# Optimization experiments

Measured on AMD Instinct MI355X. Metric: run time of the kernel, lower is better.

The kernel has to match this reference:

```python
import jax, jax.numpy as jnp
import numpy as np

NUM_TILES = 64
TPC = 8            # tiles per cluster
GRID = 16          # spline grid size
EPS = 1e-5


def setup_inputs() -> dict:
    key = jax.random.key(0)
    ks = jax.random.split(key, 6)
    B, S, D, T, DH, G = 2, 1024, 512, NUM_TILES, 128, GRID
    x = jax.random.normal(ks[0], (B, S, D), dtype=jnp.float32)
    gamma = jnp.ones((D,), jnp.float32)
    beta = jnp.zeros((D,), jnp.float32)
    # torch layouts: down.weight [DH, D], up.weight [D, DH]
    Wd = jax.random.normal(ks[1], (T, DH, D), dtype=jnp.float32) * 0.02
    spline_bases = jax.random.normal(ks[2], (T, DH, G), dtype=jnp.float32) * 0.1
    spline_slopes = jax.random.normal(ks[3], (T, DH, G), dtype=jnp.float32) * 0.1
    Wu = jax.random.normal(ks[4], (T, D, DH), dtype=jnp.float32) * 0.02
    scale = jnp.full((T,), 0.1, jnp.float32)
    return {"x": x, "gamma": gamma, "beta": beta, "Wd": Wd,
            "spline_bases": spline_bases, "spline_slopes": spline_slopes,
            "Wu": Wu, "scale": scale}


def reference(x, gamma, beta, Wd, spline_bases, spline_slopes, Wu, scale):
    B, S, D = x.shape
    T, DH, _ = Wd.shape
    C = T // TPC
    N = B * S

    # LayerNorm
    mu = x.mean(-1, keepdims=True)
    var = ((x - mu) ** 2).mean(-1, keepdims=True)
    xn = (x - mu) * jax.lax.rsqrt(var + EPS) * gamma + beta
    xf = xn.reshape(N, D)

    # Signatures (first call: ema == current tile signatures)
    tile_sigs = jnp.sign(Wd.mean(axis=1))                         # [T, D]
    cluster_sigs = jnp.sign(tile_sigs.reshape(C, TPC, D).mean(1))  # [C, D]

    # Hierarchical routing: cluster -> tile
    in_sigs = jnp.sign(xf)                                        # [N, D]
    best_c = jnp.argmax(in_sigs @ cluster_sigs.T, axis=-1)        # [N]
    tile_scores = (in_sigs @ tile_sigs.T).reshape(N, C, TPC)      # [N, C, TPC]
    sc = jnp.take_along_axis(tile_scores, best_c[:, None, None], axis=1)[:, 0, :]
    local_best = jnp.argmax(sc, axis=-1)                          # [N]
    tidx = best_c * TPC + local_best                              # [N]

    # Dispatch: gather per-token expert weights, down-project
    h = jnp.einsum('nd,nhd->nh', xf, Wd[tidx])                    # [N, DH]

    # Spline nonlinearity
    hn = jax.nn.sigmoid(h)
    idx = jnp.clip((hn * GRID).astype(jnp.int32), 0, GRID - 1)    # [N, DH]
    base = jnp.take_along_axis(spline_bases[tidx], idx[..., None], axis=-1)[..., 0]
    slope = jnp.take_along_axis(spline_slopes[tidx], idx[..., None], axis=-1)[..., 0]
    local_pos = hn * GRID - idx.astype(h.dtype)                   # (hn - idx*cell)/cell
    hs = base + slope * local_pos                                 # [N, DH]

    # Up-project, per-tile scale, combine (dropout is identity in eval)
    y = jnp.einsum('nh,ndh->nd', hs, Wu[tidx]) * scale[tidx][:, None]
    return x + y.reshape(B, S, D)
```

## Files before the change

### kernel.cpp

```cpp
#include <hip/hip_runtime.h>
#include <hip/hip_bf16.h>
#include <math.h>

#define NTILES 64
#define TPC 8
#define NCLUST 8
#define GRID_SZ 16
#define DIM 512
#define DHID 128
#define NTOK 2048
#define LN_EPS 1e-5f
#define TB 16
#define NCHUNK_MAX 192

typedef __attribute__((ext_vector_type(8))) short bf16x8;
typedef __attribute__((ext_vector_type(4))) unsigned short u16x4;
typedef __attribute__((ext_vector_type(4))) float f32x4;
typedef unsigned long long u64;

static __device__ __forceinline__ unsigned short bf16bits(float f) {
    union { __hip_bfloat16 h; unsigned short s; } u;
    u.h = __float2bfloat16(f);
    return u.s;
}

static __device__ __forceinline__ bf16x8 cvt8(const float* p) {
    float4 a = *(const float4*)p;
    float4 b = *(const float4*)(p + 4);
    float e[8] = {a.x, a.y, a.z, a.w, b.x, b.y, b.z, b.w};
    bf16x8 v;
    #pragma unroll
    for (int i = 0; i < 8; ++i) v[i] = (short)bf16bits(e[i]);
    return v;
}

static __device__ __forceinline__ u64 maj3(u64 a, u64 b, u64 c) {
    return (a & b) | (c & (a ^ b));
}

static __device__ __forceinline__ bool route_chunk(const int* counts, int lane, int cb,
                                                   int& t, int& base, int& m) {
    int cnt_l = counts[lane];
    int nck = (cnt_l + TB - 1) / TB;
    int pre = nck;
    #pragma unroll
    for (int off = 1; off < 64; off <<= 1) {
        int u = __shfl_up(pre, off);
        if (lane >= off) pre += u;
    }
    int total = __shfl(pre, 63);
    pre -= nck;
    if (cb >= total) return false;
    u64 msk = __ballot(cb >= pre && cb < pre + nck);
    t = (int)__builtin_ctzll(msk);
    base = (cb - __shfl(pre, t)) * TB;
    m = min(TB, __shfl(cnt_l, t) - base);
    return true;
}

__global__ __launch_bounds__(512) void k_prep(const float* __restrict__ x,
                                              const float* __restrict__ gamma,
                                              const float* __restrict__ beta,
                                              const float* __restrict__ Wd,
                                              const float* __restrict__ Wu,
                                              unsigned short* __restrict__ wd_b,
                                              unsigned short* __restrict__ wu_b,
                                              unsigned short* __restrict__ xn_b,
                                              u64* __restrict__ tbits,
                                              int* __restrict__ counts) {
    int bid = blockIdx.x;
    int tid = threadIdx.x;
    int lane = tid & 63;
    int wv = tid >> 6;
    if (bid < 256) {
        int t = bid >> 2, q = bid & 3;
        if (bid == 0 && tid < NTILES) counts[tid] = 0;
        int r0 = tid >> 5;
        int c4 = tid & 31;
        const float* wp = Wd + ((size_t)t * DHID + r0 * 8) * DIM + q * 128 + c4 * 4;
        unsigned short* bp = wd_b + ((size_t)t * DHID + r0 * 8) * DIM + q * 128 + c4 * 4;
        float4 v[8];
        #pragma unroll
        for (int k = 0; k < 8; ++k) v[k] = *(const float4*)(wp + (size_t)k * DIM);
        float4 a = {0.f, 0.f, 0.f, 0.f};
        #pragma unroll
        for (int k = 0; k < 8; ++k) {
            u16x4 h = {bf16bits(v[k].x), bf16bits(v[k].y), bf16bits(v[k].z), bf16bits(v[k].w)};
            *(u16x4*)(bp + (size_t)k * DIM) = h;
            a.x += v[k].x; a.y += v[k].y; a.z += v[k].z; a.w += v[k].w;
        }
        __shared__ float ps[16][128];
        *(float4*)&ps[r0][c4 * 4] = a;
        __syncthreads();
        if (tid < 128) {
            float s = 0.f;
            #pragma unroll
            for (int k = 0; k < 16; ++k) s += ps[k][tid];
            u64 b = __ballot(s < 0.f);
            if (lane == 0) tbits[t * 8 + q * 2 + wv] = b;
        }
    } else if (bid < 512) {
        int n = (bid - 256) * 8 + wv;
        const float* xr = x + (size_t)n * DIM;
        float v[8];
        float sum = 0.f;
        #pragma unroll
        for (int j = 0; j < 8; ++j) { float t = xr[lane + 64 * j]; v[j] = t; sum += t; }
        #pragma unroll
        for (int off = 32; off; off >>= 1) sum += __shfl_xor(sum, off);
        float mu = sum * (1.f / DIM);
        float sq = 0.f;
        #pragma unroll
        for (int j = 0; j < 8; ++j) { float t = v[j] - mu; sq += t * t; }
        #pragma unroll
        for (int off = 32; off; off >>= 1) sq += __shfl_xor(sq, off);
        float rs = rsqrtf(sq * (1.f / DIM) + LN_EPS);
        #pragma unroll
        for (int j = 0; j < 8; ++j) {
            int d = lane + 64 * j;
            float xv = (v[j] - mu) * rs * gamma[d] + beta[d];
            xn_b[(size_t)n * DIM + d] = bf16bits(xv);
        }
    } else {
        size_t basei = (size_t)(bid - 512) * 16384;
        #pragma unroll
        for (int k = 0; k < 4; ++k) {
            size_t off = basei + (size_t)tid * 8 + (size_t)k * 4096;
            *(bf16x8*)(wu_b + off) = cvt8(Wu + off);
        }
    }
}

__global__ __launch_bounds__(256) void k_route(const unsigned short* __restrict__ xn_b,
                                               const u64* __restrict__ tbits,
                                               int* __restrict__ counts,
                                               int* __restrict__ list) {
    int n = blockIdx.x * 4 + (threadIdx.x >> 6);
    int lane = threadIdx.x & 63;
    u64 xb[8];
    #pragma unroll
    for (int j = 0; j < 8; ++j) {
        unsigned short u = xn_b[(size_t)n * DIM + lane + 64 * j];
        xb[j] = __ballot((u & 0x8000u) != 0 && (u & 0x7fffu) != 0);
    }
    const u64* tb = tbits + lane * 8;
    int ts = 0;
    #pragma unroll
    for (int j = 0; j < 8; ++j) ts += __popcll(xb[j] ^ tb[j]);
    int tscore = DIM - 2 * ts;

    int c = lane >> 3, jw = lane & 7;
    u64 x0 = tbits[(c * TPC + 0) * 8 + jw], x1 = tbits[(c * TPC + 1) * 8 + jw];
    u64 x2 = tbits[(c * TPC + 2) * 8 + jw], x3 = tbits[(c * TPC + 3) * 8 + jw];
    u64 x4 = tbits[(c * TPC + 4) * 8 + jw], x5 = tbits[(c * TPC + 5) * 8 + jw];
    u64 x6 = tbits[(c * TPC + 6) * 8 + jw], x7 = tbits[(c * TPC + 7) * 8 + jw];
    u64 s0 = x0 ^ x1 ^ x2, c0 = maj3(x0, x1, x2);
    u64 s1 = x3 ^ x4 ^ x5, c1 = maj3(x3, x4, x5);
    u64 s2 = x6 ^ x7,      c2 = x6 & x7;
    u64 t0 = s0 ^ s1 ^ s2, t1 = maj3(s0, s1, s2);
    u64 p = c0 ^ c1, q = c0 & c1;
    u64 r = c2 ^ t1, s_ = c2 & t1;
    u64 S0 = p ^ r, car = p & r;
    u64 W0 = (q ^ s_) ^ car;
    u64 W1 = (q & s_) | (car & (q ^ s_));
    u64 cbit = W1 | (W0 & (S0 | t0));
    u64 cmsk = ~(W0 & ~W1 & ~S0 & ~t0);
    int psc = __popcll(cmsk) - 2 * __popcll((xb[jw] ^ cbit) & cmsk);
    psc += __shfl_xor(psc, 1);
    psc += __shfl_xor(psc, 2);
    psc += __shfl_xor(psc, 4);

    int bc = 0, best = __shfl(psc, 0);
    #pragma unroll
    for (int k = 1; k < NCLUST; ++k) {
        int v = __shfl(psc, k * 8);
        if (v > best) { best = v; bc = k; }
    }
    int bt = bc * TPC, bts = __shfl(tscore, bc * TPC);
    #pragma unroll
    for (int k = 1; k < TPC; ++k) {
        int v = __shfl(tscore, bc * TPC + k);
        if (v > bts) { bts = v; bt = bc * TPC + k; }
    }
    if (lane == 0) {
        int slot = atomicAdd(&counts[bt], 1);
        list[(size_t)bt * NTOK + slot] = n;
    }
}

__global__ __launch_bounds__(512, 1) void k_ffn(const float* __restrict__ x,
                                                const unsigned short* __restrict__ xn_b,
                                                const unsigned short* __restrict__ wd_b,
                                                const float* __restrict__ sb,
                                                const float* __restrict__ ss,
                                                const unsigned short* __restrict__ wu_b,
                                                const float* __restrict__ scale,
                                                const int* __restrict__ counts,
                                                const int* __restrict__ list,
                                                float* __restrict__ out) {
    int tid = threadIdx.x;
    int lane = tid & 63;
    int wv = tid >> 6;
    int cb = ((int)blockIdx.x & 7) * (NCHUNK_MAX / 8) + ((int)blockIdx.x >> 3);
    int t, base, m;
    if (!route_chunk(counts, lane, cb, t, base, m)) return;

    __shared__ __align__(16) unsigned short hsl[TB * DHID];

    int mrow = lane & 15;
    int ko = (lane >> 4) * 8;
    int tokm = list[(size_t)t * NTOK + base + min(mrow, m - 1)];

    const unsigned short* xr = xn_b + (size_t)tokm * DIM;
    const unsigned short* wr = wd_b + ((size_t)t * DHID + wv * 16 + mrow) * DIM;
    bf16x8 wreg[16], areg[16];
    #pragma unroll
    for (int kk = 0; kk < 16; ++kk) {
        int d = kk * 32 + ko;
        wreg[kk] = *(const bf16x8*)(wr + d);
        areg[kk] = *(const bf16x8*)(xr + d);
    }
    f32x4 acc0 = {0.f, 0.f, 0.f, 0.f}, acc1 = acc0;
    #pragma unroll
    for (int kk = 0; kk < 8; ++kk) {
        acc0 = __builtin_amdgcn_mfma_f32_16x16x32_bf16(areg[2 * kk], wreg[2 * kk], acc0, 0, 0, 0);
        acc1 = __builtin_amdgcn_mfma_f32_16x16x32_bf16(areg[2 * kk + 1], wreg[2 * kk + 1], acc1, 0, 0, 0);
    }
    f32x4 acc = acc0 + acc1;

    bf16x8 wupf[16];
    #pragma unroll
    for (int nt = 0; nt < 4; ++nt) {
        const unsigned short* wru = wu_b + ((size_t)t * DIM + wv * 64 + nt * 16 + mrow) * DHID;
        #pragma unroll
        for (int kk = 0; kk < 4; ++kk)
            wupf[nt * 4 + kk] = *(const bf16x8*)(wru + kk * 32 + ko);
    }

    int tokr[4];
    #pragma unroll
    for (int r = 0; r < 4; ++r) tokr[r] = __shfl(tokm, (lane >> 4) * 4 + r);
    float xpf[4][4];
    #pragma unroll
    for (int r = 0; r < 4; ++r) {
        #pragma unroll
        for (int nt = 0; nt < 4; ++nt)
            xpf[r][nt] = x[(size_t)tokr[r] * DIM + wv * 64 + nt * 16 + mrow];
    }

    int dh = wv * 16 + mrow;
    const float* sbt = sb + ((size_t)t * DHID + dh) * GRID_SZ;
    const float* sst = ss + ((size_t)t * DHID + dh) * GRID_SZ;
    #pragma unroll
    for (int r = 0; r < 4; ++r) {
        int tr = (lane >> 4) * 4 + r;
        float h = acc[r];
        float hn = 1.f / (1.f + expf(-h));
        float g = hn * (float)GRID_SZ;
        int idx = (int)g;
        idx = idx > GRID_SZ - 1 ? GRID_SZ - 1 : idx;
        float lp = g - (float)idx;
        float val = sbt[idx] + sst[idx] * lp;
        hsl[(tr * DHID + dh) ^ ((tr & 7) << 3)] = bf16bits(val);
    }
    __syncthreads();

    float sc_t = scale[t];
    bf16x8 a2[4];
    #pragma unroll
    for (int kk = 0; kk < 4; ++kk)
        a2[kk] = *(const bf16x8*)&hsl[(mrow * DHID + kk * 32 + ko) ^ ((mrow & 7) << 3)];
    #pragma unroll
    for (int nt = 0; nt < 4; ++nt) {
        int d = wv * 64 + nt * 16 + mrow;
        f32x4 au = {0.f, 0.f, 0.f, 0.f};
        #pragma unroll
        for (int kk = 0; kk < 4; ++kk)
            au = __builtin_amdgcn_mfma_f32_16x16x32_bf16(a2[kk], wupf[nt * 4 + kk], au, 0, 0, 0);
        #pragma unroll
        for (int r = 0; r < 4; ++r) {
            int tr = (lane >> 4) * 4 + r;
            if (tr < m) {
                size_t o = (size_t)tokr[r] * DIM + d;
                out[o] = xpf[r][nt] + au[r] * sc_t;
            }
        }
    }
}

extern "C" void kernel_launch(void* const* d_in, const int* in_sizes, int n_in,
                              void* d_out, int out_size, void* d_ws, size_t ws_size,
                              hipStream_t stream) {
    const float* x     = (const float*)d_in[0];
    const float* gamma = (const float*)d_in[1];
    const float* beta  = (const float*)d_in[2];
    const float* Wd    = (const float*)d_in[3];
    const float* sb    = (const float*)d_in[4];
    const float* ss    = (const float*)d_in[5];
    const float* Wu    = (const float*)d_in[6];
    const float* scale = (const float*)d_in[7];
    float* out = (float*)d_out;

    u64*   tbits         = (u64*)d_ws;
    int*   counts        = (int*)(tbits + NTILES * 8);
    int*   list          = counts + NTILES;
    unsigned short* xn_b = (unsigned short*)(list + (size_t)NTILES * NTOK);
    unsigned short* wd_b = xn_b + (size_t)NTOK * DIM;
    unsigned short* wu_b = wd_b + (size_t)NTILES * DHID * DIM;

    k_prep<<<768, 512, 0, stream>>>(x, gamma, beta, Wd, Wu, wd_b, wu_b, xn_b, tbits, counts);
    k_route<<<NTOK / 4, 256, 0, stream>>>(xn_b, tbits, counts, list);
    k_ffn<<<NCHUNK_MAX, 512, 0, stream>>>(x, xn_b, wd_b, sb, ss, wu_b, scale, counts, list, out);
}
```

Baseline: 41.89 us.

## Move Wu bf16 conversion into route kernel and precompute token sign bits in prep

The Wu fp32-to-bf16 conversion moves out of the prep kernel and into the routing kernel. Each route block loads its Wu slice up front and writes the converted bf16 after routing, so that memory traffic overlaps the latency-bound routing work. The prep kernel's LayerNorm path now emits packed sign bitmasks per token via ballot. Routing reads these 64-byte masks instead of re-reading the bf16 normalized rows. This rebalances work across kernels but raises register pressure in the route kernel from holding eight float4 values.

```diff
diff --git a/kernel.cpp b/kernel.cpp
--- a/kernel.cpp
+++ b/kernel.cpp
@@ -24,9 +24,7 @@
     return u.s;
 }
 
-static __device__ __forceinline__ bf16x8 cvt8(const float* p) {
-    float4 a = *(const float4*)p;
-    float4 b = *(const float4*)(p + 4);
+static __device__ __forceinline__ bf16x8 cvt8v(float4 a, float4 b) {
     float e[8] = {a.x, a.y, a.z, a.w, b.x, b.y, b.z, b.w};
     bf16x8 v;
     #pragma unroll
@@ -62,11 +60,10 @@
                                               const float* __restrict__ gamma,
                                               const float* __restrict__ beta,
                                               const float* __restrict__ Wd,
-                                              const float* __restrict__ Wu,
                                               unsigned short* __restrict__ wd_b,
-                                              unsigned short* __restrict__ wu_b,
                                               unsigned short* __restrict__ xn_b,
                                               u64* __restrict__ tbits,
+                                              u64* __restrict__ xbits,
                                               int* __restrict__ counts) {
     int bid = blockIdx.x;
     int tid = threadIdx.x;
@@ -99,7 +96,7 @@
             u64 b = __ballot(s < 0.f);
             if (lane == 0) tbits[t * 8 + q * 2 + wv] = b;
         }
-    } else if (bid < 512) {
+    } else {
         int n = (bid - 256) * 8 + wv;
         const float* xr = x + (size_t)n * DIM;
         float v[8];
@@ -119,30 +116,37 @@
         for (int j = 0; j < 8; ++j) {
             int d = lane + 64 * j;
             float xv = (v[j] - mu) * rs * gamma[d] + beta[d];
-            xn_b[(size_t)n * DIM + d] = bf16bits(xv);
+            unsigned short us = bf16bits(xv);
+            xn_b[(size_t)n * DIM + d] = us;
+            u64 bb = __ballot((us & 0x8000u) != 0 && (us & 0x7fffu) != 0);
+            if (lane == 0) xbits[n * 8 + j] = bb;
         }
-    } else {
-        size_t basei = (size_t)(bid - 512) * 16384;
-        #pragma unroll
-        for (int k = 0; k < 4; ++k) {
-            size_t off = basei + (size_t)tid * 8 + (size_t)k * 4096;
-            *(bf16x8*)(wu_b + off) = cvt8(Wu + off);
-        }
-    }
-}
-
-__global__ __launch_bounds__(256) void k_route(const unsigned short* __restrict__ xn_b,
+    }
+}
+
+__global__ __launch_bounds__(256) void k_route(const u64* __restrict__ xbits,
                                                const u64* __restrict__ tbits,
+                                               const float* __restrict__ Wu,
+                                               unsigned short* __restrict__ wu_b,
                                                int* __restrict__ counts,
                                                int* __restrict__ list) {
-    int n = blockIdx.x * 4 + (threadIdx.x >> 6);
-    int lane = threadIdx.x & 63;
+    int bid = blockIdx.x;
+    int tid = threadIdx.x;
+    int lane = tid & 63;
+    int wv = tid >> 6;
+
+    size_t basei = (size_t)bid * 8192 + (size_t)tid * 8;
+    float4 wl[8];
+    #pragma unroll
+    for (int k = 0; k < 4; ++k) {
+        wl[2 * k]     = *(const float4*)(Wu + basei + (size_t)k * 2048);
+        wl[2 * k + 1] = *(const float4*)(Wu + basei + (size_t)k * 2048 + 4);
+    }
+
+    int n = bid * 4 + wv;
     u64 xb[8];
     #pragma unroll
-    for (int j = 0; j < 8; ++j) {
-        unsigned short u = xn_b[(size_t)n * DIM + lane + 64 * j];
-        xb[j] = __ballot((u & 0x8000u) != 0 && (u & 0x7fffu) != 0);
-    }
+    for (int j = 0; j < 8; ++j) xb[j] = xbits[n * 8 + j];
     const u64* tb = tbits + lane * 8;
     int ts = 0;
     #pragma unroll
@@ -186,6 +190,10 @@
         int slot = atomicAdd(&counts[bt], 1);
         list[(size_t)bt * NTOK + slot] = n;
     }
+
+    #pragma unroll
+    for (int k = 0; k < 4; ++k)
+        *(bf16x8*)(wu_b + basei + (size_t)k * 2048) = cvt8v(wl[2 * k], wl[2 * k + 1]);
 }
 
 __global__ __launch_bounds__(512, 1) void k_ffn(const float* __restrict__ x,
@@ -302,13 +310,14 @@
     float* out = (float*)d_out;
 
     u64*   tbits         = (u64*)d_ws;
-    int*   counts        = (int*)(tbits + NTILES * 8);
+    u64*   xbits         = tbits + NTILES * 8;
+    int*   counts        = (int*)(xbits + (size_t)NTOK * 8);
     int*   list          = counts + NTILES;
     unsigned short* xn_b = (unsigned short*)(list + (size_t)NTILES * NTOK);
     unsigned short* wd_b = xn_b + (size_t)NTOK * DIM;
     unsigned short* wu_b = wd_b + (size_t)NTILES * DHID * DIM;
 
-    k_prep<<<768, 512, 0, stream>>>(x, gamma, beta, Wd, Wu, wd_b, wu_b, xn_b, tbits, counts);
-    k_route<<<NTOK / 4, 256, 0, stream>>>(xn_b, tbits, counts, list);
+    k_prep<<<512, 512, 0, stream>>>(x, gamma, beta, Wd, wd_b, xn_b, tbits, xbits, counts);
+    k_route<<<NTOK / 4, 256, 0, stream>>>(xbits, tbits, Wu, wu_b, counts, list);
     k_ffn<<<NCHUNK_MAX, 512, 0, stream>>>(x, xn_b, wd_b, sb, ss, wu_b, scale, counts, list, out);
 }
```

Result: slower. 43.23 us (+3.2%).
